# Kernel tuning notes

Measured on AMD Instinct MI355X. Metric: run time of the kernel, lower is better.

## Reference

```python
import jax, jax.numpy as jnp
import numpy as np
from jax import lax

BN_EPS = 1e-5
K_TOP = 2


def _conv_bn_relu_pool(x, w, b, g, beta, mean, var):
    # x: [B,C,H,W], w: [O,I,3,3]; SAME conv -> eval BN -> ReLU -> 2x2 maxpool
    y = lax.conv_general_dilated(x, w, (1, 1), 'SAME',
                                 dimension_numbers=('NCHW', 'OIHW', 'NCHW'))
    y = y + b[None, :, None, None]
    inv = g / jnp.sqrt(var + BN_EPS)
    y = (y - mean[None, :, None, None]) * inv[None, :, None, None] + beta[None, :, None, None]
    y = jax.nn.relu(y)
    return lax.reduce_window(y, -jnp.inf, lax.max, (1, 1, 2, 2), (1, 1, 2, 2), 'VALID')


def setup_inputs() -> dict:
    key = jax.random.key(0)
    ks = jax.random.split(key, 12)
    B, F_DIM, H_DIM, OUT, E = 4096, 128, 64, 10, 8
    d = {}
    d['x'] = jax.random.normal(ks[0], (B, 3, 32, 32), dtype=jnp.float32)
    # conv stacks
    def conv_block(k, cin, cout, i):
        kk = jax.random.split(k, 2)
        d[f'conv{i}_w'] = jax.random.normal(kk[0], (cout, cin, 3, 3), dtype=jnp.float32) * (1.0 / np.sqrt(cin * 9))
        d[f'conv{i}_b'] = jnp.zeros((cout,), dtype=jnp.float32)
        d[f'bn{i}_g'] = jnp.ones((cout,), dtype=jnp.float32)
        d[f'bn{i}_b'] = jnp.zeros((cout,), dtype=jnp.float32)
        d[f'bn{i}_m'] = jax.random.normal(kk[1], (cout,), dtype=jnp.float32) * 0.1
        d[f'bn{i}_v'] = jnp.ones((cout,), dtype=jnp.float32)
    conv_block(ks[1], 3, 32, 1)
    conv_block(ks[2], 32, 64, 2)
    conv_block(ks[3], 64, 128, 3)
    # experts (stacked): MLPHead Linear(128,64) -> ReLU -> Linear(64,10)
    d['w1'] = jax.random.normal(ks[4], (E, F_DIM, H_DIM), dtype=jnp.float32) * (1.0 / np.sqrt(F_DIM))
    d['b1'] = jnp.zeros((E, H_DIM), dtype=jnp.float32)
    d['w2'] = jax.random.normal(ks[5], (E, H_DIM, OUT), dtype=jnp.float32) * (1.0 / np.sqrt(H_DIM))
    d['b2'] = jnp.zeros((E, OUT), dtype=jnp.float32)
    # top-k gate: Linear(128, 8)
    d['gate_w'] = jax.random.normal(ks[6], (F_DIM, E), dtype=jnp.float32) * (1.0 / np.sqrt(F_DIM))
    d['gate_b'] = jnp.zeros((E,), dtype=jnp.float32)
    return d


def reference(x, conv1_w, conv1_b, bn1_g, bn1_b, bn1_m, bn1_v,
              conv2_w, conv2_b, bn2_g, bn2_b, bn2_m, bn2_v,
              conv3_w, conv3_b, bn3_g, bn3_b, bn3_m, bn3_v,
              w1, b1, w2, b2, gate_w, gate_b):
    # Backbone: 3x32x32 -> 128 (eval-mode BN, dropout identity)
    h = _conv_bn_relu_pool(x, conv1_w, conv1_b, bn1_g, bn1_b, bn1_m, bn1_v)  # [B,32,16,16]
    h = _conv_bn_relu_pool(h, conv2_w, conv2_b, bn2_g, bn2_b, bn2_m, bn2_v)  # [B,64,8,8]
    h = _conv_bn_relu_pool(h, conv3_w, conv3_b, bn3_g, bn3_b, bn3_m, bn3_v)  # [B,128,4,4]
    feat = jnp.mean(h, axis=(2, 3))  # AdaptiveAvgPool2d(1) + Flatten -> [B,128]

    # Top-k gate: logits -> top-k -> softmax over selected -> scatter to [B,E]
    logits = feat @ gate_w + gate_b                     # [B,E]
    vals, idx = lax.top_k(logits, K_TOP)                # [B,k]
    wk = jax.nn.softmax(vals, axis=-1)                  # [B,k]
    B, E = logits.shape
    weights = jnp.zeros((B, E), dtype=logits.dtype)
    weights = weights.at[jnp.arange(B)[:, None], idx].set(wk)

    # Dense expert MLPs (as in source), gate-weighted sum
    he = jax.nn.relu(jnp.einsum('bf,efh->beh', feat, w1) + b1[None])  # [B,E,H]
    oe = jnp.einsum('beh,eho->beo', he, w2) + b2[None]                # [B,E,O]
    return jnp.einsum('be,beo->bo', weights, oe)                      # [B,O]
```

## Files before the change

### kernel.cpp

```cpp
#include <hip/hip_runtime.h>
#include <math.h>

typedef __attribute__((ext_vector_type(8))) short short8;
typedef __attribute__((ext_vector_type(4))) float f32x4;
#define MFMA __builtin_amdgcn_mfma_f32_16x16x32_bf16

#define BN_EPS 1e-5f

static const size_t W1C2_OFF = 0;
static const size_t W2C2_OFF = 1024;
static const size_t W3C2_OFF = 19456;
static const size_t B1_OFF   = 93184;
static const size_t B2_OFF   = 93216;
static const size_t B3_OFF   = 93280;

__device__ inline unsigned short rneb(float x) {
    unsigned u = __float_as_uint(x);
    return (unsigned short)((u + 0x7FFFu + ((u >> 16) & 1u)) >> 16);
}
__device__ inline float b2f(unsigned short h) {
    return __uint_as_float(((unsigned)h) << 16);
}

__global__ __launch_bounds__(256) void k_prep(
    const float* __restrict__ c1w, const float* __restrict__ c2w, const float* __restrict__ c3w,
    const float* __restrict__ c1b, const float* __restrict__ g1, const float* __restrict__ be1,
    const float* __restrict__ m1, const float* __restrict__ v1,
    const float* __restrict__ c2b, const float* __restrict__ g2, const float* __restrict__ be2,
    const float* __restrict__ m2, const float* __restrict__ v2,
    const float* __restrict__ c3b, const float* __restrict__ g3, const float* __restrict__ be3,
    const float* __restrict__ m3, const float* __restrict__ v3,
    unsigned short* __restrict__ w1c2, unsigned short* __restrict__ w2c2,
    unsigned short* __restrict__ w3c2,
    float* __restrict__ b1c, float* __restrict__ b2c, float* __restrict__ b3c)
{
    int i = blockIdx.x * 256 + threadIdx.x;
    if (i < 2048) {
        int e = i & 7, p = (i >> 3) & 1, kc = (i >> 4) & 3, ol = (i >> 6) & 15, n = i >> 10;
        int o = n * 16 + ol, k = kc * 8 + e;
        float s = g1[o] * rsqrtf(v1[o] + BN_EPS);
        float wv = (k < 27) ? c1w[o * 27 + k] * s : 0.f;
        unsigned short h = rneb(wv);
        w1c2[i] = p ? rneb(wv - b2f(h)) : h;
        return;
    }
    i -= 2048;
    if (i < 36864) {
        int e = i & 7, p = (i >> 3) & 1, kc = (i >> 4) & 3, ol = (i >> 6) & 15;
        int n = (i >> 10) & 3, tap = i >> 12;
        int o = n * 16 + ol, ci = kc * 8 + e;
        float s = g2[o] * rsqrtf(v2[o] + BN_EPS);
        float wv = c2w[o * 288 + ci * 9 + tap] * s;
        unsigned short h = rneb(wv);
        w2c2[i] = p ? rneb(wv - b2f(h)) : h;
        return;
    }
    i -= 36864;
    if (i < 147456) {
        int e = i & 7, p = (i >> 3) & 1, kc = (i >> 4) & 3, ol = (i >> 6) & 15;
        int nf = (i >> 10) & 7, s_ = (i >> 13) & 1, tap = i >> 14;
        int o = nf * 16 + ol, ci = s_ * 32 + kc * 8 + e;
        float sc = g3[o] * rsqrtf(v3[o] + BN_EPS);
        float wv = c3w[o * 576 + ci * 9 + tap] * sc;
        unsigned short h = rneb(wv);
        w3c2[i] = p ? rneb(wv - b2f(h)) : h;
        return;
    }
    i -= 147456;
    if (i < 32) { float s = g1[i]*rsqrtf(v1[i]+BN_EPS); b1c[i] = (c1b[i]-m1[i])*s + be1[i]; return; }
    i -= 32;
    if (i < 64) { float s = g2[i]*rsqrtf(v2[i]+BN_EPS); b2c[i] = (c2b[i]-m2[i])*s + be2[i]; return; }
    i -= 64;
    if (i < 128) { float s = g3[i]*rsqrtf(v3[i]+BN_EPS); b3c[i] = (c3b[i]-m3[i])*s + be3[i]; return; }
}

__global__ __launch_bounds__(512, 4) void k_fused(
    const float* __restrict__ x,
    const unsigned short* __restrict__ w1c2,
    const unsigned short* __restrict__ w2c2,
    const unsigned short* __restrict__ w3c2,
    const float* __restrict__ b1c, const float* __restrict__ b2c, const float* __restrict__ b3c,
    const float* __restrict__ w1e, const float* __restrict__ b1e,
    const float* __restrict__ w2e, const float* __restrict__ b2e,
    const float* __restrict__ gw, const float* __restrict__ gb,
    float* __restrict__ out)
{
    __shared__ __align__(16) unsigned short R1[20736];
    __shared__ __align__(16) unsigned int   R2x[3074];
    float* sFeat = (float*)R2x;
    float* sOutB = (float*)R2x + 128;
    float* sPart = (float*)R2x + 160;

    const int b = blockIdx.x, t = threadIdx.x;
    const int lane = t & 63, w = t >> 6;
    const int l15 = lane & 15, lg = lane >> 4;
    const int4 z4 = {0, 0, 0, 0};

    {
        const float* xb = x + (size_t)b * 3072;
        for (int i = t; i < 3072; i += 512) {
            float v = xb[i];
            unsigned short h = rneb(v);
            unsigned short lo = rneb(v - b2f(h));
            R2x[i] = ((unsigned)h << 16) | lo;
        }
        if (t == 0) R2x[3072] = 0;
        for (int hh = t; hh < 272; hh += 512) {
            int pr = hh >> 2, kc = hh & 3;
            int py, px;
            if (pr < 36) { py = (pr < 18) ? 0 : 17; px = (pr < 18) ? pr : pr - 18; }
            else { int r = pr - 36; py = 1 + (r >> 1); px = (r & 1) ? 17 : 0; }
            int ei = ((py * 4 + kc) * 18 + px) * 8;
            *(int4*)(R1 + ei) = z4;
            *(int4*)(R1 + 10368 + ei) = z4;
        }
    }
    __syncthreads();

    {
        short8 b1h[2], b1l[2];
#pragma unroll
        for (int n = 0; n < 2; n++) {
            const short8* bp = (const short8*)(w1c2 + 16 * ((n * 16 + l15) * 4 + lg));
            b1h[n] = bp[0]; b1l[n] = bp[1];
        }
        int dyE[8], dxE[8], cbE[8];
#pragma unroll
        for (int e = 0; e < 8; e++) {
            int k = lg * 8 + e;
            if (k < 27) { int ci = k / 9, tp = k - ci * 9;
                          dyE[e] = tp / 3 - 1; dxE[e] = tp % 3 - 1; cbE[e] = ci << 10; }
            else { dyE[e] = -1000; dxE[e] = 0; cbE[e] = 0; }
        }
        float bia[2] = { b1c[l15], b1c[16 + l15] };
#pragma unroll 1
        for (int q = 0; q < 2; q++) {
            int m0 = 8 * w + 4 * q;
            f32x4 acc[4][2];
#pragma unroll
            for (int mi = 0; mi < 4; mi++)
#pragma unroll
                for (int n = 0; n < 2; n++) acc[mi][n] = (f32x4)0.f;
#pragma unroll
            for (int mi = 0; mi < 4; mi++) {
                int pos = 16 * (m0 + mi) + l15, py = pos >> 5, px = pos & 31;
                short8 ah, al;
#pragma unroll
                for (int e = 0; e < 8; e++) {
                    int yy = py + dyE[e], xv = px + dxE[e];
                    int idx = cbE[e] + (yy << 5) + xv;
                    bool ok = ((unsigned)yy < 32u) && ((unsigned)xv < 32u);
                    unsigned u = R2x[ok ? idx : 3072];
                    ah[e] = (short)(u >> 16);
                    al[e] = (short)(u & 0xFFFFu);
                }
#pragma unroll
                for (int n = 0; n < 2; n++) {
                    acc[mi][n] = MFMA(ah, b1h[n], acc[mi][n], 0, 0, 0);
                    acc[mi][n] = MFMA(ah, b1l[n], acc[mi][n], 0, 0, 0);
                    acc[mi][n] = MFMA(al, b1h[n], acc[mi][n], 0, 0, 0);
                }
            }
            int PY = 2 * w + q;
#pragma unroll
            for (int n = 0; n < 2; n++) {
                int o = n * 16 + l15;
#pragma unroll
                for (int h = 0; h < 2; h++)
#pragma unroll
                for (int jp = 0; jp < 2; jp++) {
                    float v00 = fmaxf(acc[h][n][2*jp]     + bia[n], 0.f);
                    float v01 = fmaxf(acc[h][n][2*jp + 1] + bia[n], 0.f);
                    float v10 = fmaxf(acc[h+2][n][2*jp]     + bia[n], 0.f);
                    float v11 = fmaxf(acc[h+2][n][2*jp + 1] + bia[n], 0.f);
                    float pm = fmaxf(fmaxf(v00, v01), fmaxf(v10, v11));
                    int PX = h * 8 + lg * 2 + jp;
                    unsigned short ph = rneb(pm), pl = rneb(pm - b2f(ph));
                    int ei = (((PY + 1) * 4 + (o >> 3)) * 18 + (PX + 1)) * 8 + (o & 7);
                    R1[ei] = ph; R1[10368 + ei] = pl;
                }
            }
        }
    }
    __syncthreads();

    {
        const int mh = w & 1, nn = w >> 1;
        f32x4 acc2[8];
#pragma unroll
        for (int mi = 0; mi < 8; mi++) acc2[mi] = (f32x4)0.f;
        const unsigned short* wb = w2c2 + ((size_t)(nn * 16 + l15) * 4 + lg) * 16;
        const int abase = (mh * 8) * 576 + lg * 144 + l15 * 8;
        short8 bhA, blA, bhB, blB;
#define LDB2(tp, BH, BL) { const short8* bp = (const short8*)(wb + (tp) * 4096); BH = bp[0]; BL = bp[1]; }
#define CMP2(tp, BH, BL) { int dy_ = (tp) / 3, dx_ = (tp) - 3 * dy_; \
        int roff_ = dy_ * 576 + dx_ * 8; \
        _Pragma("unroll") for (int mi = 0; mi < 8; mi++) { \
            int ea_ = abase + mi * 576 + roff_; \
            short8 ah_ = *(const short8*)(R1 + ea_); \
            short8 al_ = *(const short8*)(R1 + 10368 + ea_); \
            acc2[mi] = MFMA(ah_, BH, acc2[mi], 0, 0, 0); \
            acc2[mi] = MFMA(ah_, BL, acc2[mi], 0, 0, 0); \
            acc2[mi] = MFMA(al_, BH, acc2[mi], 0, 0, 0); } }
        LDB2(0, bhA, blA);
#pragma unroll 1
        for (int tp = 0; tp < 8; tp += 2) {
            LDB2(tp + 1, bhB, blB);
            CMP2(tp, bhA, blA);
            LDB2(tp + 2, bhA, blA);
            CMP2(tp + 1, bhB, blB);
        }
        CMP2(8, bhA, blA);
        __syncthreads();
        for (int hh = t; hh < 288; hh += 512) {
            int pr = hh >> 3, kc = hh & 7;
            int py, px;
            if (pr < 20) { py = (pr < 10) ? 0 : 9; px = (pr < 10) ? pr : pr - 10; }
            else { int r = pr - 20; py = 1 + (r >> 1); px = (r & 1) ? 9 : 0; }
            int ei = ((py * 8 + kc) * 11 + px) * 8;
            *(int4*)(R1 + ei) = z4;
            *(int4*)(R1 + 7040 + ei) = z4;
        }
        {
            int o = nn * 16 + l15;
            float bia = b2c[o];
#pragma unroll
            for (int mi2 = 0; mi2 < 4; mi2++) {
                int PY = mh * 4 + mi2;
#pragma unroll
                for (int jp = 0; jp < 2; jp++) {
                    float v00 = fmaxf(acc2[2*mi2][2*jp]     + bia, 0.f);
                    float v01 = fmaxf(acc2[2*mi2][2*jp + 1] + bia, 0.f);
                    float v10 = fmaxf(acc2[2*mi2+1][2*jp]     + bia, 0.f);
                    float v11 = fmaxf(acc2[2*mi2+1][2*jp + 1] + bia, 0.f);
                    float pm = fmaxf(fmaxf(v00, v01), fmaxf(v10, v11));
                    int PX = lg * 2 + jp;
                    unsigned short ph = rneb(pm), pl = rneb(pm - b2f(ph));
                    int ei = (((PY + 1) * 8 + (o >> 3)) * 11 + (PX + 1)) * 8 + (o & 7);
                    R1[ei] = ph; R1[7040 + ei] = pl;
                }
            }
        }
    }
    __syncthreads();

    {
        const int nf = w;
        f32x4 acc3[4];
#pragma unroll
        for (int mi = 0; mi < 4; mi++) acc3[mi] = (f32x4)0.f;
        const unsigned short* wb3 = w3c2 + ((size_t)(nf * 16 + l15) * 4 + lg) * 16;
        const int py0 = (l15 >> 3), px3 = l15 & 7;
        short8 bhA, blA, bhB, blB;
#define LDB3(ii, BH, BL) { const short8* bp = (const short8*)(wb3 + (ii) * 8192); BH = bp[0]; BL = bp[1]; }
#define CMP3(ii, BH, BL) { int tap_ = (ii) >> 1, s_ = (ii) & 1; \
        int dy_ = tap_ / 3, dx_ = tap_ - 3 * dy_; \
        int roff_ = dy_ * 704 + (s_ * 4 + lg) * 88 + dx_ * 8 + px3 * 8; \
        _Pragma("unroll") for (int mi = 0; mi < 4; mi++) { \
            int ea_ = (mi * 2 + py0) * 704 + roff_; \
            short8 ah_ = *(const short8*)(R1 + ea_); \
            short8 al_ = *(const short8*)(R1 + 7040 + ea_); \
            acc3[mi] = MFMA(ah_, BH, acc3[mi], 0, 0, 0); \
            acc3[mi] = MFMA(ah_, BL, acc3[mi], 0, 0, 0); \
            acc3[mi] = MFMA(al_, BH, acc3[mi], 0, 0, 0); } }
        LDB3(0, bhA, blA);
#pragma unroll 1
        for (int ii = 0; ii < 16; ii += 2) {
            LDB3(ii + 1, bhB, blB);
            CMP3(ii, bhA, blA);
            LDB3(ii + 2, bhA, blA);
            CMP3(ii + 1, bhB, blB);
        }
        LDB3(17, bhB, blB);
        CMP3(16, bhA, blA);
        CMP3(17, bhB, blB);
        {
            int o = nf * 16 + l15;
            float bia = b3c[o];
            float featsum = 0.f;
#pragma unroll
            for (int mi = 0; mi < 4; mi++) {
                float sumv = 0.f;
#pragma unroll
                for (int jp = 0; jp < 2; jp++) {
                    float v0 = fmaxf(acc3[mi][2*jp]     + bia, 0.f);
                    float v1 = fmaxf(acc3[mi][2*jp + 1] + bia, 0.f);
                    float vm = fmaxf(v0, v1);
                    vm = fmaxf(vm, __shfl_xor(vm, 32, 64));
                    sumv += vm;
                }
                sumv += __shfl_xor(sumv, 16, 64);
                featsum += sumv;
            }
            if (lane < 16) sFeat[nf * 16 + lane] = featsum * (1.0f / 16.0f);
        }
    }
    __syncthreads();

    int i1 = 0, i2 = 0;
    float wk1 = 0.f, wk2 = 0.f;
    {
        float f0 = sFeat[lane], f1 = sFeat[64 + lane];
        float lgt[8];
#pragma unroll
        for (int e = 0; e < 8; e++) {
            float p = f0 * gw[lane * 8 + e] + f1 * gw[(64 + lane) * 8 + e];
#pragma unroll
            for (int s = 1; s < 64; s <<= 1) p += __shfl_xor(p, s, 64);
            lgt[e] = p + gb[e];
        }
        float v1m = -1e30f, v2m = -1e30f;
#pragma unroll
        for (int e = 0; e < 8; e++) {
            float le = lgt[e];
            if (le > v1m) { v2m = v1m; i2 = i1; v1m = le; i1 = e; }
            else if (le > v2m) { v2m = le; i2 = e; }
        }
        float ex = expf(v2m - v1m);
        wk1 = 1.f / (1.f + ex); wk2 = ex / (1.f + ex);
        int e = (w < 4) ? i1 : i2;
        int k0 = (w & 3) * 32;
        const float* W1 = w1e + (size_t)e * 8192 + (size_t)k0 * 64;
        float hj = 0.f;
#pragma unroll 8
        for (int kk = 0; kk < 32; kk++) hj += sFeat[k0 + kk] * W1[kk * 64 + lane];
        sPart[w * 64 + lane] = hj;
    }
    __syncthreads();
    if (w < 2) {
        int e = (w == 0) ? i1 : i2;
        float wk = (w == 0) ? wk1 : wk2;
        float hj = b1e[e * 64 + lane]
                 + sPart[(w * 4 + 0) * 64 + lane] + sPart[(w * 4 + 1) * 64 + lane]
                 + sPart[(w * 4 + 2) * 64 + lane] + sPart[(w * 4 + 3) * 64 + lane];
        hj = fmaxf(hj, 0.f);
        const float* W2 = w2e + (size_t)e * 640 + lane * 10;
#pragma unroll
        for (int o = 0; o < 10; o++) {
            float po = hj * W2[o];
#pragma unroll
            for (int s = 1; s < 64; s <<= 1) po += __shfl_xor(po, s, 64);
            if (lane == 0) sOutB[w * 10 + o] = wk * (po + b2e[e * 10 + o]);
        }
    }
    __syncthreads();
    if (t < 10) out[(size_t)b * 10 + t] = sOutB[t] + sOutB[10 + t];
}

extern "C" void kernel_launch(void* const* d_in, const int* in_sizes, int n_in,
                              void* d_out, int out_size, void* d_ws, size_t ws_size,
                              hipStream_t stream)
{
    const float* x   = (const float*)d_in[0];
    const float* c1w = (const float*)d_in[1];
    const float* c1b = (const float*)d_in[2];
    const float* g1  = (const float*)d_in[3];
    const float* be1 = (const float*)d_in[4];
    const float* m1  = (const float*)d_in[5];
    const float* v1  = (const float*)d_in[6];
    const float* c2w = (const float*)d_in[7];
    const float* c2b = (const float*)d_in[8];
    const float* g2  = (const float*)d_in[9];
    const float* be2 = (const float*)d_in[10];
    const float* m2  = (const float*)d_in[11];
    const float* v2  = (const float*)d_in[12];
    const float* c3w = (const float*)d_in[13];
    const float* c3b = (const float*)d_in[14];
    const float* g3  = (const float*)d_in[15];
    const float* be3 = (const float*)d_in[16];
    const float* m3  = (const float*)d_in[17];
    const float* v3  = (const float*)d_in[18];
    const float* w1e = (const float*)d_in[19];
    const float* b1e = (const float*)d_in[20];
    const float* w2e = (const float*)d_in[21];
    const float* b2e = (const float*)d_in[22];
    const float* gw  = (const float*)d_in[23];
    const float* gb  = (const float*)d_in[24];

    float* ws = (float*)d_ws;
    unsigned short* w1c2 = (unsigned short*)(ws + W1C2_OFF);
    unsigned short* w2c2 = (unsigned short*)(ws + W2C2_OFF);
    unsigned short* w3c2 = (unsigned short*)(ws + W3C2_OFF);
    float* b1c = ws + B1_OFF;
    float* b2c = ws + B2_OFF;
    float* b3c = ws + B3_OFF;

    k_prep<<<729, 256, 0, stream>>>(c1w, c2w, c3w,
                                    c1b, g1, be1, m1, v1,
                                    c2b, g2, be2, m2, v2,
                                    c3b, g3, be3, m3, v3,
                                    w1c2, w2c2, w3c2, b1c, b2c, b3c);
    k_fused<<<4096, 512, 0, stream>>>(x, w1c2, w2c2, w3c2, b1c, b2c, b3c,
                                      w1e, b1e, w2e, b2e, gw, gb, (float*)d_out);
}
```

Baseline: 295.2 us.

## Drop padded LDS halos, use unpadded layouts with predicated zero-source loads

Replaces the halo-padded LDS activation buffers with compact unpadded layouts in one shared array. Out-of-range taps now load from a zeroed slot, and whole rows are skipped in conv2, so the border zeroing loops go away. This also shrinks the LDS footprint, which may allow more resident blocks. The cost is extra index and predicate arithmetic in the inner loops, and the unpadded strides may cause LDS bank conflicts.

Result: slower. 310.0 us (+5.0%).

```diff
diff --git a/kernel.cpp b/kernel.cpp
--- a/kernel.cpp
+++ b/kernel.cpp
@@ -85,11 +85,11 @@
     const float* __restrict__ gw, const float* __restrict__ gb,
     float* __restrict__ out)
 {
-    __shared__ __align__(16) unsigned short R1[20736];
-    __shared__ __align__(16) unsigned int   R2x[3074];
-    float* sFeat = (float*)R2x;
-    float* sOutB = (float*)R2x + 128;
-    float* sPart = (float*)R2x + 160;
+    __shared__ __align__(16) unsigned short LDSU[24576];
+    unsigned int* xs = (unsigned int*)(LDSU + 16384);
+    float* sFeat = (float*)LDSU;
+    float* sPart = (float*)LDSU + 256;
+    float* sOutB = (float*)LDSU + 768;
 
     const int b = blockIdx.x, t = threadIdx.x;
     const int lane = t & 63, w = t >> 6;
@@ -102,18 +102,9 @@
             float v = xb[i];
             unsigned short h = rneb(v);
             unsigned short lo = rneb(v - b2f(h));
-            R2x[i] = ((unsigned)h << 16) | lo;
-        }
-        if (t == 0) R2x[3072] = 0;
-        for (int hh = t; hh < 272; hh += 512) {
-            int pr = hh >> 2, kc = hh & 3;
-            int py, px;
-            if (pr < 36) { py = (pr < 18) ? 0 : 17; px = (pr < 18) ? pr : pr - 18; }
-            else { int r = pr - 36; py = 1 + (r >> 1); px = (r & 1) ? 17 : 0; }
-            int ei = ((py * 4 + kc) * 18 + px) * 8;
-            *(int4*)(R1 + ei) = z4;
-            *(int4*)(R1 + 10368 + ei) = z4;
-        }
+            xs[4 + i] = ((unsigned)h << 16) | lo;
+        }
+        if (t < 4) xs[t] = 0;
     }
     __syncthreads();
 
@@ -150,7 +141,7 @@
                     int yy = py + dyE[e], xv = px + dxE[e];
                     int idx = cbE[e] + (yy << 5) + xv;
                     bool ok = ((unsigned)yy < 32u) && ((unsigned)xv < 32u);
-                    unsigned u = R2x[ok ? idx : 3072];
+                    unsigned u = xs[ok ? idx + 4 : 0];
                     ah[e] = (short)(u >> 16);
                     al[e] = (short)(u & 0xFFFFu);
                 }
@@ -175,9 +166,9 @@
                     float v11 = fmaxf(acc[h+2][n][2*jp + 1] + bia[n], 0.f);
                     float pm = fmaxf(fmaxf(v00, v01), fmaxf(v10, v11));
                     int PX = h * 8 + lg * 2 + jp;
-                    unsigned short ph = rneb(pm), pl = rneb(pm - b2f(ph));
-                    int ei = (((PY + 1) * 4 + (o >> 3)) * 18 + (PX + 1)) * 8 + (o & 7);
-                    R1[ei] = ph; R1[10368 + ei] = pl;
+                    int ei = PY * 512 + (o >> 3) * 128 + PX * 8 + (o & 7);
+                    LDSU[ei] = rneb(pm);
+                    LDSU[8192 + ei] = rneb(pm - b2f(rneb(pm)));
                 }
             }
         }
@@ -190,18 +181,20 @@
 #pragma unroll
         for (int mi = 0; mi < 8; mi++) acc2[mi] = (f32x4)0.f;
         const unsigned short* wb = w2c2 + ((size_t)(nn * 16 + l15) * 4 + lg) * 16;
-        const int abase = (mh * 8) * 576 + lg * 144 + l15 * 8;
         short8 bhA, blA, bhB, blB;
 #define LDB2(tp, BH, BL) { const short8* bp = (const short8*)(wb + (tp) * 4096); BH = bp[0]; BL = bp[1]; }
-#define CMP2(tp, BH, BL) { int dy_ = (tp) / 3, dx_ = (tp) - 3 * dy_; \
-        int roff_ = dy_ * 576 + dx_ * 8; \
+#define CMP2(tp, BH, BL) { const int dy_ = (tp) / 3, dx_ = (tp) - 3 * dy_; \
+        const int pxp_ = l15 + dx_ - 1; \
+        const bool okc_ = ((unsigned)pxp_ < 16u); \
         _Pragma("unroll") for (int mi = 0; mi < 8; mi++) { \
-            int ea_ = abase + mi * 576 + roff_; \
-            short8 ah_ = *(const short8*)(R1 + ea_); \
-            short8 al_ = *(const short8*)(R1 + 10368 + ea_); \
-            acc2[mi] = MFMA(ah_, BH, acc2[mi], 0, 0, 0); \
-            acc2[mi] = MFMA(ah_, BL, acc2[mi], 0, 0, 0); \
-            acc2[mi] = MFMA(al_, BH, acc2[mi], 0, 0, 0); } }
+            int py1_ = mh * 8 + mi + dy_ - 1; \
+            if ((unsigned)py1_ < 16u) { \
+                int ea_ = py1_ * 512 + lg * 128 + pxp_ * 8; \
+                short8 ah_ = *(const short8*)(LDSU + (okc_ ? ea_ : 16384)); \
+                short8 al_ = *(const short8*)(LDSU + (okc_ ? ea_ + 8192 : 16384)); \
+                acc2[mi] = MFMA(ah_, BH, acc2[mi], 0, 0, 0); \
+                acc2[mi] = MFMA(ah_, BL, acc2[mi], 0, 0, 0); \
+                acc2[mi] = MFMA(al_, BH, acc2[mi], 0, 0, 0); } } }
         LDB2(0, bhA, blA);
 #pragma unroll 1
         for (int tp = 0; tp < 8; tp += 2) {
@@ -212,15 +205,7 @@
         }
         CMP2(8, bhA, blA);
         __syncthreads();
-        for (int hh = t; hh < 288; hh += 512) {
-            int pr = hh >> 3, kc = hh & 7;
-            int py, px;
-            if (pr < 20) { py = (pr < 10) ? 0 : 9; px = (pr < 10) ? pr : pr - 10; }
-            else { int r = pr - 20; py = 1 + (r >> 1); px = (r & 1) ? 9 : 0; }
-            int ei = ((py * 8 + kc) * 11 + px) * 8;
-            *(int4*)(R1 + ei) = z4;
-            *(int4*)(R1 + 7040 + ei) = z4;
-        }
+        if (t == 0) *(int4*)((char*)LDSU + 592) = z4;
         {
             int o = nn * 16 + l15;
             float bia = b2c[o];
@@ -235,9 +220,9 @@
                     float v11 = fmaxf(acc2[2*mi2+1][2*jp + 1] + bia, 0.f);
                     float pm = fmaxf(fmaxf(v00, v01), fmaxf(v10, v11));
                     int PX = lg * 2 + jp;
-                    unsigned short ph = rneb(pm), pl = rneb(pm - b2f(ph));
-                    int ei = (((PY + 1) * 8 + (o >> 3)) * 11 + (PX + 1)) * 8 + (o & 7);
-                    R1[ei] = ph; R1[7040 + ei] = pl;
+                    int ei = PY * 512 + (o >> 3) * 64 + PX * 8 + (o & 7);
+                    LDSU[16384 + ei] = rneb(pm);
+                    LDSU[20480 + ei] = rneb(pm - b2f(rneb(pm)));
                 }
             }
         }
@@ -253,13 +238,16 @@
         const int py0 = (l15 >> 3), px3 = l15 & 7;
         short8 bhA, blA, bhB, blB;
 #define LDB3(ii, BH, BL) { const short8* bp = (const short8*)(wb3 + (ii) * 8192); BH = bp[0]; BL = bp[1]; }
-#define CMP3(ii, BH, BL) { int tap_ = (ii) >> 1, s_ = (ii) & 1; \
-        int dy_ = tap_ / 3, dx_ = tap_ - 3 * dy_; \
-        int roff_ = dy_ * 704 + (s_ * 4 + lg) * 88 + dx_ * 8 + px3 * 8; \
+#define CMP3(ii, BH, BL) { const int tap_ = (ii) >> 1, s_ = (ii) & 1; \
+        const int dy_ = tap_ / 3, dx_ = tap_ - 3 * dy_; \
+        const int pxp_ = px3 + dx_ - 1; \
+        const bool okc_ = ((unsigned)pxp_ < 8u); \
         _Pragma("unroll") for (int mi = 0; mi < 4; mi++) { \
-            int ea_ = (mi * 2 + py0) * 704 + roff_; \
-            short8 ah_ = *(const short8*)(R1 + ea_); \
-            short8 al_ = *(const short8*)(R1 + 7040 + ea_); \
+            int py1_ = mi * 2 + py0 + dy_ - 1; \
+            bool ok_ = ((unsigned)py1_ < 8u) && okc_; \
+            int ea_ = py1_ * 512 + (s_ * 4 + lg) * 64 + pxp_ * 8; \
+            short8 ah_ = *(const short8*)(LDSU + (ok_ ? 16384 + ea_ : 296)); \
+            short8 al_ = *(const short8*)(LDSU + (ok_ ? 20480 + ea_ : 296)); \
             acc3[mi] = MFMA(ah_, BH, acc3[mi], 0, 0, 0); \
             acc3[mi] = MFMA(ah_, BL, acc3[mi], 0, 0, 0); \
             acc3[mi] = MFMA(al_, BH, acc3[mi], 0, 0, 0); } }
```

## Pre-pack input into bf16 hi/lo words globally and gather conv1 from global

Applied to the files above, without the earlier changes.

Adds a separate kernel that converts the whole input into packed bf16 hi/lo pairs in a workspace buffer. The fused kernel then gathers conv1 operands directly from global/L2 instead of staging the image in LDS, which removes the staging loop, one barrier and the separate LDS array, and drops the occupancy hint from the launch bounds. The cost is an extra full pass writing and reading a 48MB buffer, plus uncoalesced global gathers in conv1 in place of LDS reads.

Result: slower. 327.5 us (+11.0%).

```diff
diff --git a/kernel.cpp b/kernel.cpp
--- a/kernel.cpp
+++ b/kernel.cpp
@@ -13,6 +13,7 @@
 static const size_t B1_OFF   = 93184;
 static const size_t B2_OFF   = 93216;
 static const size_t B3_OFF   = 93280;
+static const size_t PXP_OFF  = 93440;
 
 __device__ inline unsigned short rneb(float x) {
     unsigned u = __float_as_uint(x);
@@ -20,6 +21,10 @@
 }
 __device__ inline float b2f(unsigned short h) {
     return __uint_as_float(((unsigned)h) << 16);
+}
+__device__ inline unsigned packhl(float v) {
+    unsigned short h = rneb(v);
+    return ((unsigned)h << 16) | (unsigned)rneb(v - b2f(h));
 }
 
 __global__ __launch_bounds__(256) void k_prep(
@@ -74,8 +79,19 @@
     if (i < 128) { float s = g3[i]*rsqrtf(v3[i]+BN_EPS); b3c[i] = (c3b[i]-m3[i])*s + be3[i]; return; }
 }
 
-__global__ __launch_bounds__(512, 4) void k_fused(
-    const float* __restrict__ x,
+__global__ __launch_bounds__(256) void k_packx(const float* __restrict__ x,
+                                               unsigned* __restrict__ pxg)
+{
+    size_t gid = (size_t)blockIdx.x * 256 + threadIdx.x;
+    float4 v = ((const float4*)x)[gid];
+    uint4 o;
+    o.x = packhl(v.x); o.y = packhl(v.y); o.z = packhl(v.z); o.w = packhl(v.w);
+    ((uint4*)pxg)[gid] = o;
+    if (gid < 64) pxg[12582912 + gid] = 0;
+}
+
+__global__ __launch_bounds__(512) void k_fused(
+    const unsigned* __restrict__ pxp,
     const unsigned short* __restrict__ w1c2,
     const unsigned short* __restrict__ w2c2,
     const unsigned short* __restrict__ w3c2,
@@ -85,37 +101,25 @@
     const float* __restrict__ gw, const float* __restrict__ gb,
     float* __restrict__ out)
 {
-    __shared__ __align__(16) unsigned short R1[20736];
-    __shared__ __align__(16) unsigned int   R2x[3074];
-    float* sFeat = (float*)R2x;
-    float* sOutB = (float*)R2x + 128;
-    float* sPart = (float*)R2x + 160;
+    __shared__ __align__(16) unsigned short LDSU[20736];
+    float* sFeat = (float*)(LDSU + 14080);
+    float* sPart = (float*)(LDSU + 14336);
+    float* sOutB = (float*)(LDSU + 15360);
 
     const int b = blockIdx.x, t = threadIdx.x;
     const int lane = t & 63, w = t >> 6;
     const int l15 = lane & 15, lg = lane >> 4;
     const int4 z4 = {0, 0, 0, 0};
 
-    {
-        const float* xb = x + (size_t)b * 3072;
-        for (int i = t; i < 3072; i += 512) {
-            float v = xb[i];
-            unsigned short h = rneb(v);
-            unsigned short lo = rneb(v - b2f(h));
-            R2x[i] = ((unsigned)h << 16) | lo;
-        }
-        if (t == 0) R2x[3072] = 0;
-        for (int hh = t; hh < 272; hh += 512) {
-            int pr = hh >> 2, kc = hh & 3;
-            int py, px;
-            if (pr < 36) { py = (pr < 18) ? 0 : 17; px = (pr < 18) ? pr : pr - 18; }
-            else { int r = pr - 36; py = 1 + (r >> 1); px = (r & 1) ? 17 : 0; }
-            int ei = ((py * 4 + kc) * 18 + px) * 8;
-            *(int4*)(R1 + ei) = z4;
-            *(int4*)(R1 + 10368 + ei) = z4;
-        }
-    }
-    __syncthreads();
+    for (int hh = t; hh < 272; hh += 512) {
+        int pr = hh >> 2, kc = hh & 3;
+        int py, px;
+        if (pr < 36) { py = (pr < 18) ? 0 : 17; px = (pr < 18) ? pr : pr - 18; }
+        else { int r = pr - 36; py = 1 + (r >> 1); px = (r & 1) ? 17 : 0; }
+        int ei = ((py * 4 + kc) * 18 + px) * 8;
+        *(int4*)(LDSU + ei) = z4;
+        *(int4*)(LDSU + 10368 + ei) = z4;
+    }
 
     {
         short8 b1h[2], b1l[2];
@@ -133,6 +137,7 @@
             else { dyE[e] = -1000; dxE[e] = 0; cbE[e] = 0; }
         }
         float bia[2] = { b1c[l15], b1c[16 + l15] };
+        const unsigned* gxb = pxp + (size_t)b * 3072;
 #pragma unroll 1
         for (int q = 0; q < 2; q++) {
             int m0 = 8 * w + 4 * q;
@@ -150,7 +155,8 @@
                     int yy = py + dyE[e], xv = px + dxE[e];
                     int idx = cbE[e] + (yy << 5) + xv;
                     bool ok = ((unsigned)yy < 32u) && ((unsigned)xv < 32u);
-                    unsigned u = R2x[ok ? idx : 3072];
+                    unsigned u = gxb[idx];
+                    u = ok ? u : 0u;
                     ah[e] = (short)(u >> 16);
                     al[e] = (short)(u & 0xFFFFu);
                 }
@@ -177,7 +183,7 @@
                     int PX = h * 8 + lg * 2 + jp;
                     unsigned short ph = rneb(pm), pl = rneb(pm - b2f(ph));
                     int ei = (((PY + 1) * 4 + (o >> 3)) * 18 + (PX + 1)) * 8 + (o & 7);
-                    R1[ei] = ph; R1[10368 + ei] = pl;
+                    LDSU[ei] = ph; LDSU[10368 + ei] = pl;
                 }
             }
         }
@@ -197,8 +203,8 @@
         int roff_ = dy_ * 576 + dx_ * 8; \
         _Pragma("unroll") for (int mi = 0; mi < 8; mi++) { \
             int ea_ = abase + mi * 576 + roff_; \
-            short8 ah_ = *(const short8*)(R1 + ea_); \
-            short8 al_ = *(const short8*)(R1 + 10368 + ea_); \
+            short8 ah_ = *(const short8*)(LDSU + ea_); \
+            short8 al_ = *(const short8*)(LDSU + 10368 + ea_); \
             acc2[mi] = MFMA(ah_, BH, acc2[mi], 0, 0, 0); \
             acc2[mi] = MFMA(ah_, BL, acc2[mi], 0, 0, 0); \
             acc2[mi] = MFMA(al_, BH, acc2[mi], 0, 0, 0); } }
@@ -218,8 +224,8 @@
             if (pr < 20) { py = (pr < 10) ? 0 : 9; px = (pr < 10) ? pr : pr - 10; }
             else { int r = pr - 20; py = 1 + (r >> 1); px = (r & 1) ? 9 : 0; }
             int ei = ((py * 8 + kc) * 11 + px) * 8;
-            *(int4*)(R1 + ei) = z4;
-            *(int4*)(R1 + 7040 + ei) = z4;
+            *(int4*)(LDSU + ei) = z4;
+            *(int4*)(LDSU + 7040 + ei) = z4;
         }
         {
             int o = nn * 16 + l15;
@@ -237,7 +243,7 @@
                     int PX = lg * 2 + jp;
                     unsigned short ph = rneb(pm), pl = rneb(pm - b2f(ph));
                     int ei = (((PY + 1) * 8 + (o >> 3)) * 11 + (PX + 1)) * 8 + (o & 7);
-                    R1[ei] = ph; R1[7040 + ei] = pl;
+                    LDSU[ei] = ph; LDSU[7040 + ei] = pl;
                 }
             }
         }
@@ -258,8 +264,8 @@
         int roff_ = dy_ * 704 + (s_ * 4 + lg) * 88 + dx_ * 8 + px3 * 8; \
         _Pragma("unroll") for (int mi = 0; mi < 4; mi++) { \
             int ea_ = (mi * 2 + py0) * 704 + roff_; \
-            short8 ah_ = *(const short8*)(R1 + ea_); \
-            short8 al_ = *(const short8*)(R1 + 7040 + ea_); \
+            short8 ah_ = *(const short8*)(LDSU + ea_); \
+            short8 al_ = *(const short8*)(LDSU + 7040 + ea_); \
             acc3[mi] = MFMA(ah_, BH, acc3[mi], 0, 0, 0); \
             acc3[mi] = MFMA(ah_, BL, acc3[mi], 0, 0, 0); \
             acc3[mi] = MFMA(al_, BH, acc3[mi], 0, 0, 0); } }
@@ -384,12 +390,14 @@
     float* b1c = ws + B1_OFF;
     float* b2c = ws + B2_OFF;
     float* b3c = ws + B3_OFF;
+    unsigned* pxp = (unsigned*)(ws + PXP_OFF);
 
     k_prep<<<729, 256, 0, stream>>>(c1w, c2w, c3w,
                                     c1b, g1, be1, m1, v1,
                                     c2b, g2, be2, m2, v2,
                                     c3b, g3, be3, m3, v3,
                                     w1c2, w2c2, w3c2, b1c, b2c, b3c);
-    k_fused<<<4096, 512, 0, stream>>>(x, w1c2, w2c2, w3c2, b1c, b2c, b3c,
+    k_packx<<<12288, 256, 0, stream>>>(x, pxp);
+    k_fused<<<4096, 512, 0, stream>>>(pxp, w1c2, w2c2, w3c2, b1c, b2c, b3c,
                                       w1e, b1e, w2e, b2e, gw, gb, (float*)d_out);
 }
```

## Switch conv2 and conv3 to 32x32x16 MFMA tiles with repacked weights

Applied to the files above, without the earlier changes.

Conv2 and conv3 now use the 32x32x16 bf16 MFMA instead of 16x16x32, and the weight prep packing changes to match the new B-fragment layout. Each warp gets larger output tiles, so operand reuse per LDS load improves and fewer MFMA instructions are issued. Conv3 splits the spatial M dimension across two warp groups, which needs an extra shared-memory reduction and barrier for the pooled features. Risks are more accumulator registers per warp and changed LDS bank access patterns.

After: 304.9 us. 3.3% more time.

```diff
diff --git a/kernel.cpp b/kernel.cpp
--- a/kernel.cpp
+++ b/kernel.cpp
@@ -3,7 +3,9 @@
 
 typedef __attribute__((ext_vector_type(8))) short short8;
 typedef __attribute__((ext_vector_type(4))) float f32x4;
-#define MFMA __builtin_amdgcn_mfma_f32_16x16x32_bf16
+typedef __attribute__((ext_vector_type(16))) float f32x16;
+#define MFMA16 __builtin_amdgcn_mfma_f32_16x16x32_bf16
+#define MFMA32 __builtin_amdgcn_mfma_f32_32x32x16_bf16
 
 #define BN_EPS 1e-5f
 
@@ -46,9 +48,9 @@
     }
     i -= 2048;
     if (i < 36864) {
-        int e = i & 7, p = (i >> 3) & 1, kc = (i >> 4) & 3, ol = (i >> 6) & 15;
-        int n = (i >> 10) & 3, tap = i >> 12;
-        int o = n * 16 + ol, ci = kc * 8 + e;
+        int e = i & 7, p = (i >> 3) & 1, kh = (i >> 4) & 1, col = (i >> 5) & 31;
+        int nt = (i >> 10) & 1, ks = (i >> 11) & 1, tap = i >> 12;
+        int o = nt * 32 + col, ci = ks * 16 + kh * 8 + e;
         float s = g2[o] * rsqrtf(v2[o] + BN_EPS);
         float wv = c2w[o * 288 + ci * 9 + tap] * s;
         unsigned short h = rneb(wv);
@@ -57,9 +59,9 @@
     }
     i -= 36864;
     if (i < 147456) {
-        int e = i & 7, p = (i >> 3) & 1, kc = (i >> 4) & 3, ol = (i >> 6) & 15;
-        int nf = (i >> 10) & 7, s_ = (i >> 13) & 1, tap = i >> 14;
-        int o = nf * 16 + ol, ci = s_ * 32 + kc * 8 + e;
+        int e = i & 7, p = (i >> 3) & 1, kh = (i >> 4) & 1, col = (i >> 5) & 31;
+        int nf = (i >> 10) & 3, ks = (i >> 12) & 3, tap = i >> 14;
+        int o = nf * 32 + col, ci = ks * 16 + kh * 8 + e;
         float sc = g3[o] * rsqrtf(v3[o] + BN_EPS);
         float wv = c3w[o * 576 + ci * 9 + tap] * sc;
         unsigned short h = rneb(wv);
@@ -87,9 +89,9 @@
 {
     __shared__ __align__(16) unsigned short R1[20736];
     __shared__ __align__(16) unsigned int   R2x[3074];
-    float* sFeat = (float*)R2x;
-    float* sOutB = (float*)R2x + 128;
-    float* sPart = (float*)R2x + 160;
+    float* sFeatP = (float*)R2x;
+    float* sPart  = (float*)R2x + 256;
+    float* sOutB  = (float*)R2x + 768;
 
     const int b = blockIdx.x, t = threadIdx.x;
     const int lane = t & 63, w = t >> 6;
@@ -156,9 +158,9 @@
                 }
 #pragma unroll
                 for (int n = 0; n < 2; n++) {
-                    acc[mi][n] = MFMA(ah, b1h[n], acc[mi][n], 0, 0, 0);
-                    acc[mi][n] = MFMA(ah, b1l[n], acc[mi][n], 0, 0, 0);
-                    acc[mi][n] = MFMA(al, b1h[n], acc[mi][n], 0, 0, 0);
+                    acc[mi][n] = MFMA16(ah, b1h[n], acc[mi][n], 0, 0, 0);
+                    acc[mi][n] = MFMA16(ah, b1l[n], acc[mi][n], 0, 0, 0);
+                    acc[mi][n] = MFMA16(al, b1h[n], acc[mi][n], 0, 0, 0);
                 }
             }
             int PY = 2 * w + q;
@@ -185,122 +187,126 @@
     __syncthreads();
 
     {
-        const int mh = w & 1, nn = w >> 1;
-        f32x4 acc2[8];
-#pragma unroll
-        for (int mi = 0; mi < 8; mi++) acc2[mi] = (f32x4)0.f;
-        const unsigned short* wb = w2c2 + ((size_t)(nn * 16 + l15) * 4 + lg) * 16;
-        const int abase = (mh * 8) * 576 + lg * 144 + l15 * 8;
+        const int nt = w & 1, wm = w >> 1;
+        const int r = lane & 31, kh = lane >> 5;
+        f32x16 acc2A = (f32x16)0.f, acc2B = (f32x16)0.f;
+        const unsigned short* wb = w2c2 + ((size_t)(nt * 32 + r) * 2 + kh) * 16;
+        const int pyb0 = 2 * (2 * wm)     + (r >> 4);
+        const int pyb1 = 2 * (2 * wm + 1) + (r >> 4);
+        const int pxb = r & 15;
         short8 bhA, blA, bhB, blB;
-#define LDB2(tp, BH, BL) { const short8* bp = (const short8*)(wb + (tp) * 4096); BH = bp[0]; BL = bp[1]; }
-#define CMP2(tp, BH, BL) { int dy_ = (tp) / 3, dx_ = (tp) - 3 * dy_; \
-        int roff_ = dy_ * 576 + dx_ * 8; \
-        _Pragma("unroll") for (int mi = 0; mi < 8; mi++) { \
-            int ea_ = abase + mi * 576 + roff_; \
-            short8 ah_ = *(const short8*)(R1 + ea_); \
-            short8 al_ = *(const short8*)(R1 + 10368 + ea_); \
-            acc2[mi] = MFMA(ah_, BH, acc2[mi], 0, 0, 0); \
-            acc2[mi] = MFMA(ah_, BL, acc2[mi], 0, 0, 0); \
-            acc2[mi] = MFMA(al_, BH, acc2[mi], 0, 0, 0); } }
-        LDB2(0, bhA, blA);
+#define LDBW2(u, BH, BL) { const short8* bp = (const short8*)(wb + (u) * 2048); BH = bp[0]; BL = bp[1]; }
+#define CMPW2(u, BH, BL) { const int tap_ = (u) >> 1, ks_ = (u) & 1; \
+        const int dy_ = tap_ / 3, dx_ = tap_ - 3 * dy_; \
+        const int kc_ = ks_ * 2 + kh; \
+        const int co_ = (kc_ * 18 + pxb + dx_) * 8; \
+        { int ea_ = (pyb0 + dy_) * 576 + co_; \
+          short8 ah_ = *(const short8*)(R1 + ea_); \
+          short8 al_ = *(const short8*)(R1 + 10368 + ea_); \
+          acc2A = MFMA32(ah_, BH, acc2A, 0, 0, 0); \
+          acc2A = MFMA32(ah_, BL, acc2A, 0, 0, 0); \
+          acc2A = MFMA32(al_, BH, acc2A, 0, 0, 0); } \
+        { int ea_ = (pyb1 + dy_) * 576 + co_; \
+          short8 ah_ = *(const short8*)(R1 + ea_); \
+          short8 al_ = *(const short8*)(R1 + 10368 + ea_); \
+          acc2B = MFMA32(ah_, BH, acc2B, 0, 0, 0); \
+          acc2B = MFMA32(ah_, BL, acc2B, 0, 0, 0); \
+          acc2B = MFMA32(al_, BH, acc2B, 0, 0, 0); } }
+        LDBW2(0, bhA, blA);
 #pragma unroll 1
-        for (int tp = 0; tp < 8; tp += 2) {
-            LDB2(tp + 1, bhB, blB);
-            CMP2(tp, bhA, blA);
-            LDB2(tp + 2, bhA, blA);
-            CMP2(tp + 1, bhB, blB);
-        }
-        CMP2(8, bhA, blA);
+        for (int u = 0; u < 16; u += 2) {
+            LDBW2(u + 1, bhB, blB);
+            CMPW2(u, bhA, blA);
+            LDBW2(u + 2, bhA, blA);
+            CMPW2(u + 1, bhB, blB);
+        }
+        LDBW2(17, bhB, blB);
+        CMPW2(16, bhA, blA);
+        CMPW2(17, bhB, blB);
         __syncthreads();
         for (int hh = t; hh < 288; hh += 512) {
             int pr = hh >> 3, kc = hh & 7;
             int py, px;
             if (pr < 20) { py = (pr < 10) ? 0 : 9; px = (pr < 10) ? pr : pr - 10; }
-            else { int r = pr - 20; py = 1 + (r >> 1); px = (r & 1) ? 9 : 0; }
+            else { int rr = pr - 20; py = 1 + (rr >> 1); px = (rr & 1) ? 9 : 0; }
             int ei = ((py * 8 + kc) * 11 + px) * 8;
             *(int4*)(R1 + ei) = z4;
             *(int4*)(R1 + 7040 + ei) = z4;
         }
         {
-            int o = nn * 16 + l15;
-            float bia = b2c[o];
-#pragma unroll
-            for (int mi2 = 0; mi2 < 4; mi2++) {
-                int PY = mh * 4 + mi2;
-#pragma unroll
-                for (int jp = 0; jp < 2; jp++) {
-                    float v00 = fmaxf(acc2[2*mi2][2*jp]     + bia, 0.f);
-                    float v01 = fmaxf(acc2[2*mi2][2*jp + 1] + bia, 0.f);
-                    float v10 = fmaxf(acc2[2*mi2+1][2*jp]     + bia, 0.f);
-                    float v11 = fmaxf(acc2[2*mi2+1][2*jp + 1] + bia, 0.f);
-                    float pm = fmaxf(fmaxf(v00, v01), fmaxf(v10, v11));
-                    int PX = lg * 2 + jp;
-                    unsigned short ph = rneb(pm), pl = rneb(pm - b2f(ph));
-                    int ei = (((PY + 1) * 8 + (o >> 3)) * 11 + (PX + 1)) * 8 + (o & 7);
-                    R1[ei] = ph; R1[7040 + ei] = pl;
-                }
+            int oc = nt * 32 + r;
+            float bia = b2c[oc];
+#define EPI2(ACC, MT) { \
+            _Pragma("unroll") for (int g = 0; g < 4; g++) { \
+                float v0 = fmaxf(ACC[2*g]     + bia, 0.f); \
+                float v1 = fmaxf(ACC[2*g + 1] + bia, 0.f); \
+                float v2 = fmaxf(ACC[2*g + 8] + bia, 0.f); \
+                float v3 = fmaxf(ACC[2*g + 9] + bia, 0.f); \
+                float pm = fmaxf(fmaxf(v0, v1), fmaxf(v2, v3)); \
+                int PX = (g & 1) + (g >> 1) * 4 + kh * 2; \
+                int ei = ((((MT) + 1) * 8 + (oc >> 3)) * 11 + (PX + 1)) * 8 + (oc & 7); \
+                unsigned short ph = rneb(pm); \
+                R1[ei] = ph; R1[7040 + ei] = rneb(pm - b2f(ph)); } }
+            EPI2(acc2A, 2 * wm);
+            EPI2(acc2B, 2 * wm + 1);
+        }
+    }
+    __syncthreads();
+
+    {
+        const int mt = w >> 2, nf = w & 3;
+        const int r = lane & 31, kh = lane >> 5;
+        f32x16 acc3 = (f32x16)0.f;
+        const unsigned short* wb3 = w3c2 + ((size_t)(nf * 32 + r) * 2 + kh) * 16;
+        const int pyb = mt * 4 + (r >> 3), pxb = r & 7;
+        short8 bhA, blA, bhB, blB;
+#define LDBW3(u, BH, BL) { const short8* bp = (const short8*)(wb3 + (u) * 4096); BH = bp[0]; BL = bp[1]; }
+#define CMPW3(u, BH, BL) { const int tap_ = (u) >> 2, ks_ = (u) & 3; \
+        const int dy_ = tap_ / 3, dx_ = tap_ - 3 * dy_; \
+        const int kc_ = ks_ * 2 + kh; \
+        int ea_ = (((pyb + dy_) * 8 + kc_) * 11 + (pxb + dx_)) * 8; \
+        short8 ah_ = *(const short8*)(R1 + ea_); \
+        short8 al_ = *(const short8*)(R1 + 7040 + ea_); \
+        acc3 = MFMA32(ah_, BH, acc3, 0, 0, 0); \
+        acc3 = MFMA32(ah_, BL, acc3, 0, 0, 0); \
+        acc3 = MFMA32(al_, BH, acc3, 0, 0, 0); }
+        LDBW3(0, bhA, blA);
+#pragma unroll 1
+        for (int u = 0; u < 34; u += 2) {
+            LDBW3(u + 1, bhB, blB);
+            CMPW3(u, bhA, blA);
+            LDBW3(u + 2, bhA, blA);
+            CMPW3(u + 1, bhB, blB);
+        }
+        LDBW3(35, bhB, blB);
+        CMPW3(34, bhA, blA);
+        CMPW3(35, bhB, blB);
+        {
+            int oc = nf * 32 + r;
+            float bia = b3c[oc];
+            float fs = 0.f;
+#pragma unroll
+            for (int pl = 0; pl < 2; pl++)
+#pragma unroll
+            for (int g = 0; g < 2; g++) {
+                float v0 = fmaxf(acc3[pl*8 + 2*g]     + bia, 0.f);
+                float v1 = fmaxf(acc3[pl*8 + 2*g + 1] + bia, 0.f);
+                float v2 = fmaxf(acc3[pl*8 + 2*g + 4] + bia, 0.f);
+                float v3 = fmaxf(acc3[pl*8 + 2*g + 5] + bia, 0.f);
+                fs += fmaxf(fmaxf(v0, v1), fmaxf(v2, v3));
             }
-        }
-    }
-    __syncthreads();
-
-    {
-        const int nf = w;
-        f32x4 acc3[4];
-#pragma unroll
-        for (int mi = 0; mi < 4; mi++) acc3[mi] = (f32x4)0.f;
-        const unsigned short* wb3 = w3c2 + ((size_t)(nf * 16 + l15) * 4 + lg) * 16;
-        const int py0 = (l15 >> 3), px3 = l15 & 7;
-        short8 bhA, blA, bhB, blB;
-#define LDB3(ii, BH, BL) { const short8* bp = (const short8*)(wb3 + (ii) * 8192); BH = bp[0]; BL = bp[1]; }
-#define CMP3(ii, BH, BL) { int tap_ = (ii) >> 1, s_ = (ii) & 1; \
-        int dy_ = tap_ / 3, dx_ = tap_ - 3 * dy_; \
-        int roff_ = dy_ * 704 + (s_ * 4 + lg) * 88 + dx_ * 8 + px3 * 8; \
-        _Pragma("unroll") for (int mi = 0; mi < 4; mi++) { \
-            int ea_ = (mi * 2 + py0) * 704 + roff_; \
-            short8 ah_ = *(const short8*)(R1 + ea_); \
-            short8 al_ = *(const short8*)(R1 + 7040 + ea_); \
-            acc3[mi] = MFMA(ah_, BH, acc3[mi], 0, 0, 0); \
-            acc3[mi] = MFMA(ah_, BL, acc3[mi], 0, 0, 0); \
-            acc3[mi] = MFMA(al_, BH, acc3[mi], 0, 0, 0); } }
-        LDB3(0, bhA, blA);
-#pragma unroll 1
-        for (int ii = 0; ii < 16; ii += 2) {
-            LDB3(ii + 1, bhB, blB);
-            CMP3(ii, bhA, blA);
-            LDB3(ii + 2, bhA, blA);
-            CMP3(ii + 1, bhB, blB);
-        }
-        LDB3(17, bhB, blB);
-        CMP3(16, bhA, blA);
-        CMP3(17, bhB, blB);
-        {
-            int o = nf * 16 + l15;
-            float bia = b3c[o];
-            float featsum = 0.f;
-#pragma unroll
-            for (int mi = 0; mi < 4; mi++) {
-                float sumv = 0.f;
-#pragma unroll
-                for (int jp = 0; jp < 2; jp++) {
-                    float v0 = fmaxf(acc3[mi][2*jp]     + bia, 0.f);
-                    float v1 = fmaxf(acc3[mi][2*jp + 1] + bia, 0.f);
-                    float vm = fmaxf(v0, v1);
-                    vm = fmaxf(vm, __shfl_xor(vm, 32, 64));
-                    sumv += vm;
-                }
-                sumv += __shfl_xor(sumv, 16, 64);
-                featsum += sumv;
-            }
-            if (lane < 16) sFeat[nf * 16 + lane] = featsum * (1.0f / 16.0f);
-        }
-    }
+            fs += __shfl_xor(fs, 32, 64);
+            if (lane < 32) sFeatP[mt * 128 + oc] = fs;
+        }
+    }
+    __syncthreads();
+    if (t < 128) sFeatP[t] = (sFeatP[t] + sFeatP[128 + t]) * (1.0f / 16.0f);
     __syncthreads();
 
     int i1 = 0, i2 = 0;
     float wk1 = 0.f, wk2 = 0.f;
     {
-        float f0 = sFeat[lane], f1 = sFeat[64 + lane];
+        float f0 = sFeatP[lane], f1 = sFeatP[64 + lane];
         float lgt[8];
 #pragma unroll
         for (int e = 0; e < 8; e++) {
@@ -323,7 +329,7 @@
         const float* W1 = w1e + (size_t)e * 8192 + (size_t)k0 * 64;
         float hj = 0.f;
 #pragma unroll 8
-        for (int kk = 0; kk < 32; kk++) hj += sFeat[k0 + kk] * W1[kk * 64 + lane];
+        for (int kk = 0; kk < 32; kk++) hj += sFeatP[k0 + kk] * W1[kk * 64 + lane];
         sPart[w * 64 + lane] = hj;
     }
     __syncthreads();
```
